# Performance work log

Measured on AMD Instinct MI355X. Metric: run time of the kernel, lower is better.

Reference implementation:

```python
import jax, jax.numpy as jnp
import numpy as np

EPS = 1e-10  # faithful to original: masked scores are set to eps, not -inf


def setup_inputs() -> dict:
    key = jax.random.key(0)
    ks = jax.random.split(key, 5)
    B, S, D, N, H = 2, 2048, 1024, 16, 64
    init_range = 0.02
    residual = jax.random.normal(ks[0], (B, S, D), dtype=jnp.float32)
    W_key = jax.random.normal(ks[1], (N, D, H), dtype=jnp.float32) * init_range
    W_query = jax.random.normal(ks[2], (N, D, H), dtype=jnp.float32) * init_range
    W_values = jax.random.normal(ks[3], (N, D, H), dtype=jnp.float32) * init_range
    W_output = jax.random.normal(ks[4], (N, H, D), dtype=jnp.float32) * init_range
    return {
        "residual": residual,
        "W_key": W_key, "W_query": W_query, "W_values": W_values, "W_output": W_output,
        "Bias_key": jnp.zeros((N, H), jnp.float32),
        "Bias_query": jnp.zeros((N, H), jnp.float32),
        "Bias_values": jnp.zeros((N, H), jnp.float32),
        "Bias_output": jnp.zeros((D,), jnp.float32),
    }


def reference(residual, W_key, W_query, W_values, W_output,
              Bias_key, Bias_query, Bias_values, Bias_output):
    B, S, D = residual.shape
    N, _, H = W_key.shape
    # projections: [b,s,n,h]
    keys = jnp.einsum('bse,neh->bsnh', residual, W_key) + Bias_key
    queries = jnp.einsum('bse,neh->bsnh', residual, W_query) + Bias_query
    values = jnp.einsum('bse,neh->bsnh', residual, W_values) + Bias_values
    # scores: [b,n,q,k]
    scores = jnp.einsum('bknh,bqnh->bnqk', keys, queries) / jnp.sqrt(jnp.asarray(H, scores_dtype(residual)))
    q_idx = jnp.arange(S)[:, None]
    k_idx = jnp.arange(S)[None, :]
    causal_mask = q_idx < k_idx  # future positions
    # QUIRK of original module: masked scores are assigned eps (~0), not -inf
    scores = jnp.where(causal_mask[None, None, :, :], jnp.asarray(EPS, scores.dtype), scores)
    probs = jax.nn.softmax(scores, axis=3)
    weighted = jnp.einsum('bnqk,bknh->bqnh', probs, values)
    out = jnp.einsum('bqnh,nhe->bqe', weighted, W_output) + Bias_output
    return out


def scores_dtype(x):
    return x.dtype
```

## Files before the change

kernel.cpp:

```cpp
#include <hip/hip_runtime.h>
#include <hip/hip_bf16.h>
#include <cmath>

typedef __bf16 bf16;
typedef __attribute__((ext_vector_type(4))) __bf16 bf16x4;
typedef __attribute__((ext_vector_type(8))) __bf16 bf16x8;
typedef __attribute__((ext_vector_type(4))) float f32x4;

#define B_ 2
#define S_ 2048
#define D_ 1024
#define N_ 16
#define H_ 64
#define LOG2E 1.44269504088896340736f

__device__ __forceinline__ void gload16(const bf16* g, bf16* l) {
  __builtin_amdgcn_global_load_lds(
      (const __attribute__((address_space(1))) void*)(g),
      (__attribute__((address_space(3))) void*)(l), 16, 0, 0);
}

__device__ __forceinline__ f32x4 mfma16(bf16x8 a, bf16x8 b, f32x4 c) {
  return __builtin_amdgcn_mfma_f32_16x16x32_bf16(a, b, c, 0, 0, 0);
}

__device__ __forceinline__ f32x4 zero4() {
  f32x4 v = {0.0f, 0.0f, 0.0f, 0.0f};
  return v;
}

__global__ __launch_bounds__(256) void cvt_kernel(
    const float* __restrict__ in, bf16* __restrict__ out, int n8) {
  int id = blockIdx.x * 256 + threadIdx.x;
  if (id >= n8) return;
  const float4* p = (const float4*)(in + (size_t)id * 8);
  float4 v0 = p[0], v1 = p[1];
  bf16x8 o;
  o[0] = (bf16)v0.x; o[1] = (bf16)v0.y; o[2] = (bf16)v0.z; o[3] = (bf16)v0.w;
  o[4] = (bf16)v1.x; o[5] = (bf16)v1.y; o[6] = (bf16)v1.z; o[7] = (bf16)v1.w;
  *(bf16x8*)(out + (size_t)id * 8) = o;
}

__global__ __launch_bounds__(256) void qkvw_transpose_kernel(
    const float* __restrict__ Wk, const float* __restrict__ Wq,
    const float* __restrict__ Wv, bf16* __restrict__ out) {
  __shared__ bf16 t[64][72];
  const int z = blockIdx.z;
  const float* W = (z < 16) ? Wk : (z < 32) ? Wq : Wv;
  const float* ing = W + (size_t)(z & 15) * (1024 * 64);
  bf16* outg = out + (size_t)z * (64 * 1024);
  const int r0 = blockIdx.x * 64;
  const int t8 = threadIdx.x & 7, trow = threadIdx.x >> 3;
#pragma unroll
  for (int p = 0; p < 2; ++p) {
    int r = trow + p * 32;
    const float4* src = (const float4*)(ing + (size_t)(r0 + r) * 64 + t8 * 8);
    float4 v0 = src[0], v1 = src[1];
    bf16x8 o;
    o[0] = (bf16)v0.x; o[1] = (bf16)v0.y; o[2] = (bf16)v0.z; o[3] = (bf16)v0.w;
    o[4] = (bf16)v1.x; o[5] = (bf16)v1.y; o[6] = (bf16)v1.z; o[7] = (bf16)v1.w;
    *(bf16x8*)(&t[r][t8 * 8]) = o;
  }
  __syncthreads();
#pragma unroll
  for (int p = 0; p < 2; ++p) {
    int c = trow + p * 32;
    bf16x8 v;
#pragma unroll
    for (int j = 0; j < 8; ++j) v[j] = t[t8 * 8 + j][c];
    *(bf16x8*)(outg + (size_t)c * 1024 + r0 + t8 * 8) = v;
  }
}

__global__ __launch_bounds__(256) void transpose_f32bf16_kernel(
    const float* __restrict__ in, bf16* __restrict__ out, int R, int C) {
  __shared__ bf16 t[64][72];
  const size_t mat = (size_t)R * C;
  const float* ing = in + (size_t)blockIdx.z * mat;
  bf16* outg = out + (size_t)blockIdx.z * mat;
  const int r0 = blockIdx.x * 64, c0 = blockIdx.y * 64;
  const int t8 = threadIdx.x & 7, trow = threadIdx.x >> 3;
#pragma unroll
  for (int p = 0; p < 2; ++p) {
    int r = trow + p * 32;
    const float4* src = (const float4*)(ing + (size_t)(r0 + r) * C + c0 + t8 * 8);
    float4 v0 = src[0], v1 = src[1];
    bf16x8 o;
    o[0] = (bf16)v0.x; o[1] = (bf16)v0.y; o[2] = (bf16)v0.z; o[3] = (bf16)v0.w;
    o[4] = (bf16)v1.x; o[5] = (bf16)v1.y; o[6] = (bf16)v1.z; o[7] = (bf16)v1.w;
    *(bf16x8*)(&t[r][t8 * 8]) = o;
  }
  __syncthreads();
#pragma unroll
  for (int p = 0; p < 2; ++p) {
    int c = trow + p * 32;
    bf16x8 v;
#pragma unroll
    for (int j = 0; j < 8; ++j) v[j] = t[t8 * 8 + j][c];
    *(bf16x8*)(outg + (size_t)(c0 + c) * R + r0 + t8 * 8) = v;
  }
}

__global__ __launch_bounds__(256) void transpose_bf16_kernel(
    const bf16* __restrict__ in, bf16* __restrict__ out, int R, int C) {
  __shared__ bf16 t[64][72];
  const size_t mat = (size_t)R * C;
  const bf16* ing = in + (size_t)blockIdx.z * mat;
  bf16* outg = out + (size_t)blockIdx.z * mat;
  const int r0 = blockIdx.x * 64, c0 = blockIdx.y * 64;
  const int t8 = threadIdx.x & 7, trow = threadIdx.x >> 3;
#pragma unroll
  for (int p = 0; p < 2; ++p) {
    int r = trow + p * 32;
    bf16x8 v = *(const bf16x8*)(ing + (size_t)(r0 + r) * C + c0 + t8 * 8);
    *(bf16x8*)(&t[r][t8 * 8]) = v;
  }
  __syncthreads();
#pragma unroll
  for (int p = 0; p < 2; ++p) {
    int c = trow + p * 32;
    bf16x8 v;
#pragma unroll
    for (int j = 0; j < 8; ++j) v[j] = t[t8 * 8 + j][c];
    *(bf16x8*)(outg + (size_t)(c0 + c) * R + r0 + t8 * 8) = v;
  }
}

__global__ __launch_bounds__(256) void sufv_tot_kernel(
    const bf16* __restrict__ Vp, float* __restrict__ tot) {
  __shared__ float red[4][64];
  const int hd = blockIdx.x, seg = blockIdx.y;
  const int h = threadIdx.x & 63, sub = threadIdx.x >> 6;
  const bf16* Vh = Vp + (size_t)hd * S_ * H_;
  float a = 0.0f;
  const int k0 = seg * 32 + sub * 8;
#pragma unroll
  for (int k = 0; k < 8; ++k) a += (float)Vh[(size_t)(k0 + k) * H_ + h];
  red[sub][h] = a;
  __syncthreads();
  if (sub == 0)
    tot[(hd * 64 + seg) * 64 + h] = red[0][h] + red[1][h] + red[2][h] + red[3][h];
}

__global__ __launch_bounds__(64) void sufv_scan_kernel(
    bf16* __restrict__ VS, const float* __restrict__ tot) {
  const int hd = blockIdx.x, seg = blockIdx.y, h = threadIdx.x;
  bf16* Vh = VS + (size_t)hd * S_ * H_;
  float a = 0.0f;
  for (int s2 = seg + 1; s2 < 64; ++s2) a += tot[(hd * 64 + s2) * 64 + h];
  for (int k = seg * 32 + 31; k >= seg * 32; --k) {
    const float v = (float)Vh[(size_t)k * H_ + h];
    Vh[(size_t)k * H_ + h] = (bf16)a;
    a += v;
  }
}

__global__ __launch_bounds__(512) void gemm_proj_kernel(
    const bf16* __restrict__ A, const bf16* __restrict__ Bt,
    const float* __restrict__ bk, const float* __restrict__ bq,
    const float* __restrict__ bv, bf16* __restrict__ proj_base) {
  __shared__ bf16 As[2][2][256 * 32];
  __shared__ bf16 Bs[2][2][256 * 32];
  const int tid = threadIdx.x;
  const int w = tid >> 6, l = tid & 63, lan = l & 15, grp = l >> 4;
  const int wm128 = (w >> 2) * 128, wn64 = (w & 3) * 64;
  const int m0 = blockIdx.y * 256, n0 = blockIdx.x * 256;
  const int zc = n0 >> 10;
  const float* bias = (zc == 0) ? bk : (zc == 1 ? bq : bv);
  bf16* Out = proj_base + (size_t)zc * ((size_t)B_ * N_ * S_ * H_);
  const int posx = (grp ^ ((lan >> 1) & 3)) << 3;

#define STG(LDS_, GP_, rb_, buf_, kh_, kb_)                                    \
  do {                                                                         \
    _Pragma("unroll") for (int jj = 0; jj < 2; ++jj) {                         \
      const int ci = jj * 512 + tid;                                           \
      const int rw = ci >> 2, cp = ci & 3;                                     \
      const int gg = cp ^ ((rw >> 1) & 3);                                     \
      gload16(GP_ + (size_t)((rb_) + rw) * 1024 + (kb_) + (kh_) * 32 + gg * 8, \
              &LDS_[buf_][kh_][(jj * 512 + w * 64) * 8]);                      \
    }                                                                          \
  } while (0)

  f32x4 acc[8][4];
#pragma unroll
  for (int i = 0; i < 8; ++i)
#pragma unroll
    for (int jv = 0; jv < 4; ++jv) acc[i][jv] = zero4();

  bf16x8 b[4];

#define DO_PHASE(buf_, mq_, kk_, READB_)                                       \
  do {                                                                         \
    if (READB_) {                                                              \
      _Pragma("unroll") for (int nf = 0; nf < 4; ++nf)                         \
        b[nf] = *(const bf16x8*)(&Bs[buf_][kk_][(wn64 + nf * 16 + lan) * 32 + posx]); \
    }                                                                          \
    bf16x8 a[4];                                                               \
    _Pragma("unroll") for (int mf = 0; mf < 4; ++mf)                           \
      a[mf] = *(const bf16x8*)(&As[buf_][kk_][(wm128 + (mq_) * 64 + mf * 16 + lan) * 32 + posx]); \
    __builtin_amdgcn_s_setprio(1);                                             \
    _Pragma("unroll") for (int mf = 0; mf < 4; ++mf)                           \
      _Pragma("unroll") for (int nf = 0; nf < 4; ++nf)                         \
        acc[(mq_) * 4 + mf][nf] = mfma16(a[mf], b[nf], acc[(mq_) * 4 + mf][nf]); \
    __builtin_amdgcn_s_setprio(0);                                             \
  } while (0)

  STG(As, A, m0, 0, 0, 0);
  STG(Bs, Bt, n0, 0, 0, 0);
  STG(As, A, m0, 0, 1, 0);
  STG(Bs, Bt, n0, 0, 1, 0);

  for (int t = 0; t < 15; ++t) {
    const int buf = t & 1;
    const int nkb = (t + 1) * 64;
    STG(As, A, m0, buf ^ 1, 0, nkb);
    asm volatile("s_waitcnt vmcnt(6)" ::: "memory");
    __builtin_amdgcn_s_barrier();
    asm volatile("" ::: "memory");
    DO_PHASE(buf, 0, 0, true);
    STG(Bs, Bt, n0, buf ^ 1, 0, nkb);
    asm volatile("" ::: "memory");
    __builtin_amdgcn_s_barrier();
    asm volatile("" ::: "memory");
    DO_PHASE(buf, 1, 0, false);
    STG(As, A, m0, buf ^ 1, 1, nkb);
    asm volatile("s_waitcnt vmcnt(6)" ::: "memory");
    __builtin_amdgcn_s_barrier();
    asm volatile("" ::: "memory");
    DO_PHASE(buf, 0, 1, true);
    STG(Bs, Bt, n0, buf ^ 1, 1, nkb);
    asm volatile("" ::: "memory");
    __builtin_amdgcn_s_barrier();
    asm volatile("" ::: "memory");
    DO_PHASE(buf, 1, 1, false);
  }
  {
    asm volatile("s_waitcnt vmcnt(4)" ::: "memory");
    __builtin_amdgcn_s_barrier();
    asm volatile("" ::: "memory");
    DO_PHASE(1, 0, 0, true);
    DO_PHASE(1, 1, 0, false);
    asm volatile("s_waitcnt vmcnt(0)" ::: "memory");
    __builtin_amdgcn_s_barrier();
    asm volatile("" ::: "memory");
    DO_PHASE(1, 0, 1, true);
    DO_PHASE(1, 1, 1, false);
  }
#undef STG
#undef DO_PHASE

#pragma unroll
  for (int nf = 0; nf < 4; ++nf) {
    const int c10 = (n0 + wn64 + nf * 16 + lan) & 1023;
    const float bs = bias[c10];
    const int n = c10 >> 6, h = c10 & 63;
#pragma unroll
    for (int am = 0; am < 8; ++am) {
#pragma unroll
      for (int r = 0; r < 4; ++r) {
        const int m = m0 + wm128 + am * 16 + grp * 4 + r;
        const int bb = m >> 11, s = m & 2047;
        Out[((size_t)((bb * N_ + n) * S_ + s)) * H_ + h] = (bf16)(acc[am][nf][r] + bs);
      }
    }
  }
}

__global__ __launch_bounds__(256) void gemm_out_kernel(
    const bf16* __restrict__ A, const bf16* __restrict__ Bt,
    const float* __restrict__ bias, float* __restrict__ Out) {
  __shared__ bf16 As[128 * 64];
  __shared__ bf16 Bs[128 * 64];
  const int tid = threadIdx.x;
  const int w = tid >> 6, l = tid & 63, lan = l & 15, grp = l >> 4;
  const int mb = (w >> 1) * 64, nb = (w & 1) * 64;
  const int m0 = blockIdx.y * 128, n0 = blockIdx.x * 128;
  const int lrow8 = l >> 3;
  const int swl = ((l & 7) ^ lrow8) * 8;
  const int l7 = lan & 7;

  f32x4 acc[4][4];
#pragma unroll
  for (int i = 0; i < 4; ++i)
#pragma unroll
    for (int j = 0; j < 4; ++j) acc[i][j] = zero4();

  for (int kb = 0; kb < 1024; kb += 64) {
    __syncthreads();
#pragma unroll
    for (int i = 0; i < 4; ++i) {
      int ch = w * 4 + i;
      gload16(A + (size_t)(m0 + ch * 8 + lrow8) * 1024 + kb + swl, As + ch * 512);
      gload16(Bt + (size_t)(n0 + ch * 8 + lrow8) * 1024 + kb + swl, Bs + ch * 512);
    }
    __syncthreads();
#pragma unroll
    for (int kk = 0; kk < 2; ++kk) {
      bf16x8 a[4], b[4];
#pragma unroll
      for (int mf = 0; mf < 4; ++mf)
        a[mf] = *(const bf16x8*)(As + (mb + mf * 16 + lan) * 64 + (((grp + kk * 4) ^ l7) << 3));
#pragma unroll
      for (int nf = 0; nf < 4; ++nf)
        b[nf] = *(const bf16x8*)(Bs + (nb + nf * 16 + lan) * 64 + (((grp + kk * 4) ^ l7) << 3));
#pragma unroll
      for (int mf = 0; mf < 4; ++mf)
#pragma unroll
        for (int nf = 0; nf < 4; ++nf)
          acc[mf][nf] = mfma16(a[mf], b[nf], acc[mf][nf]);
    }
  }
#pragma unroll
  for (int nf = 0; nf < 4; ++nf) {
    int c = n0 + nb + nf * 16 + lan;
    float bs = bias[c];
#pragma unroll
    for (int mf = 0; mf < 4; ++mf) {
#pragma unroll
      for (int r = 0; r < 4; ++r) {
        int m = m0 + mb + mf * 16 + grp * 4 + r;
        Out[(size_t)m * 1024 + c] = acc[mf][nf][r] + bs;
      }
    }
  }
}

__global__ __launch_bounds__(256) void attn_kernel(
    const bf16* __restrict__ Qp, const bf16* __restrict__ Kp,
    const bf16* __restrict__ Vt, const bf16* __restrict__ Suf,
    bf16* __restrict__ Wtd, float* __restrict__ PoA, float* __restrict__ PoB,
    float* __restrict__ PpA, float* __restrict__ PpB) {
  __shared__ bf16 Ks[2][64 * 64];
  __shared__ bf16 Vs[2][64 * 64];
  __shared__ bf16 Ps[4][32 * 72];
  const int tid = threadIdx.x;
  const int w = tid >> 6, l = tid & 63, lan = l & 15, grp = l >> 4;
  const int bi = blockIdx.x;
  const int qq = bi >> 8;
  const int j = bi & 255;
  const int hd = j & 31, wv = j >> 5;
  int x, t0, t1;
  if (qq == 0)      { x = 15 - wv; t0 = 0;     t1 = x + 1; }
  else if (qq == 1) { x = 15 - wv; t0 = x + 1; t1 = 2 * x + 2; }
  else              { x = wv;      t0 = 0;     t1 = 2 * x + 2; }
  const int qw = x * 128 + w * 32;
  const bf16* Qh = Qp + (size_t)hd * S_ * H_;
  const bf16* Kh = Kp + (size_t)hd * S_ * H_;
  const bf16* Vh = Vt + (size_t)hd * H_ * S_;
  const bf16* Sufh = Suf + (size_t)hd * S_ * H_;
  const int lrow8 = l >> 3;
  const int swl = ((l & 7) ^ lrow8) * 8;
  const int l7 = lan & 7;
  const float cexp = 0.125f * LOG2E;

#define STAGE(buf, kb_)                                                        \
  do {                                                                         \
    _Pragma("unroll") for (int i2 = 0; i2 < 2; ++i2) {                         \
      int ch = w * 2 + i2;                                                     \
      gload16(Kh + (size_t)((kb_) + ch * 8 + lrow8) * H_ + swl,                \
              &Ks[buf][ch * 512]);                                             \
      gload16(Vh + (size_t)(ch * 8 + lrow8) * S_ + (kb_) + swl,                \
              &Vs[buf][ch * 512]);                                             \
    }                                                                          \
  } while (0)

  bf16x8 qa[2][2];
#pragma unroll
  for (int qt = 0; qt < 2; ++qt)
#pragma unroll
    for (int kf = 0; kf < 2; ++kf)
      qa[qt][kf] = *(const bf16x8*)(Qh + (size_t)(qw + qt * 16 + lan) * H_ + grp * 8 + kf * 32);

  f32x4 o[2][4];
  float psum[2] = {0.0f, 0.0f};
#pragma unroll
  for (int qt = 0; qt < 2; ++qt)
#pragma unroll
    for (int hf = 0; hf < 4; ++hf) o[qt][hf] = zero4();

  bf16* Pw = &Ps[w][0];

  STAGE(0, t0 * 64);
  for (int tt = t0; tt < t1; ++tt) {
    const int kb = tt * 64;
    const int cur = (tt - t0) & 1;
    if (tt + 1 < t1) {
      STAGE(cur ^ 1, kb + 64);
      asm volatile("s_waitcnt vmcnt(4)" ::: "memory");
    } else {
      asm volatile("s_waitcnt vmcnt(0)" ::: "memory");
    }
    __builtin_amdgcn_s_barrier();

    if (kb <= qw + 31) {
      const bf16* Kc = &Ks[cur][0];
      const bf16* Vc = &Vs[cur][0];

      f32x4 s2[4][2];
#pragma unroll
      for (int k2 = 0; k2 < 4; ++k2)
#pragma unroll
        for (int qt = 0; qt < 2; ++qt) s2[k2][qt] = zero4();
      __builtin_amdgcn_s_setprio(1);
#pragma unroll
      for (int kf = 0; kf < 2; ++kf) {
        bf16x8 kfr[4];
#pragma unroll
        for (int k2 = 0; k2 < 4; ++k2)
          kfr[k2] = *(const bf16x8*)(Kc + (k2 * 16 + lan) * 64 + (((grp + kf * 4) ^ l7) << 3));
#pragma unroll
        for (int k2 = 0; k2 < 4; ++k2)
#pragma unroll
          for (int qt = 0; qt < 2; ++qt)
            s2[k2][qt] = mfma16(kfr[k2], qa[qt][kf], s2[k2][qt]);
      }
      __builtin_amdgcn_s_setprio(0);

      const bool maskt = (kb + 63 > qw);
#pragma unroll
      for (int qt = 0; qt < 2; ++qt) {
        const int q_g = qw + qt * 16 + lan;
#pragma unroll
        for (int k2 = 0; k2 < 4; ++k2) {
          f32x4 p;
#pragma unroll
          for (int r = 0; r < 4; ++r) p[r] = exp2f(s2[k2][qt][r] * cexp);
          if (maskt) {
            const int kg0 = kb + k2 * 16 + grp * 4;
#pragma unroll
            for (int r = 0; r < 4; ++r)
              if (kg0 + r > q_g) p[r] = 0.0f;
          }
          psum[qt] += (p[0] + p[1]) + (p[2] + p[3]);
          unsigned plo, phi;
          asm("v_cvt_pk_bf16_f32 %0, %1, %2" : "=v"(plo) : "v"(p[0]), "v"(p[1]));
          asm("v_cvt_pk_bf16_f32 %0, %1, %2" : "=v"(phi) : "v"(p[2]), "v"(p[3]));
          uint2 u; u.x = plo; u.y = phi;
          *(uint2*)(Pw + (qt * 16 + lan) * 72 + k2 * 16 + grp * 4) = u;
        }
      }

      __builtin_amdgcn_s_setprio(1);
#pragma unroll
      for (int ks = 0; ks < 2; ++ks) {
        bf16x8 pa[2], vb[4];
#pragma unroll
        for (int qt = 0; qt < 2; ++qt)
          pa[qt] = *(const bf16x8*)(Pw + (qt * 16 + lan) * 72 + grp * 8 + ks * 32);
#pragma unroll
        for (int hf = 0; hf < 4; ++hf)
          vb[hf] = *(const bf16x8*)(Vc + (hf * 16 + lan) * 64 + (((grp + ks * 4) ^ l7) << 3));
#pragma unroll
        for (int qt = 0; qt < 2; ++qt)
#pragma unroll
          for (int hf = 0; hf < 4; ++hf)
            o[qt][hf] = mfma16(pa[qt], vb[hf], o[qt][hf]);
      }
      __builtin_amdgcn_s_setprio(0);
    }
    __builtin_amdgcn_s_barrier();
  }
#undef STAGE

#pragma unroll
  for (int qt = 0; qt < 2; ++qt) {
    psum[qt] += __shfl_xor(psum[qt], 16);
    psum[qt] += __shfl_xor(psum[qt], 32);
  }

  if (qq == 2) {
    const size_t outbase = (size_t)(hd >> 4) * S_ * (N_ * H_) + (size_t)(hd & 15) * H_;
#pragma unroll
    for (int qt = 0; qt < 2; ++qt) {
#pragma unroll
      for (int r = 0; r < 4; ++r) {
        const int q_g = qw + qt * 16 + grp * 4 + r;
        const float ps = __shfl(psum[qt], grp * 4 + r);
        const float inv = 1.0f / (ps + (float)(2047 - q_g));
#pragma unroll
        for (int hf = 0; hf < 4; ++hf) {
          const int h = hf * 16 + lan;
          const float suf = (float)Sufh[(size_t)q_g * H_ + h];
          Wtd[outbase + (size_t)q_g * (N_ * H_) + h] = (bf16)((o[qt][hf][r] + suf) * inv);
        }
      }
    }
  } else {
    float* Po = (qq == 0) ? PoA : PoB;
    float* Pp = (qq == 0) ? PpA : PpB;
    const int pb = (hd * 8 + (x - 8)) * 128 + w * 32;
#pragma unroll
    for (int qt = 0; qt < 2; ++qt) {
#pragma unroll
      for (int r = 0; r < 4; ++r) {
        const int rl = qt * 16 + grp * 4 + r;
        const float ps = __shfl(psum[qt], grp * 4 + r);
        if (lan == 0) Pp[pb + rl] = ps;
#pragma unroll
        for (int hf = 0; hf < 4; ++hf)
          Po[(size_t)(pb + rl) * 64 + hf * 16 + lan] = o[qt][hf][r];
      }
    }
  }
}

__global__ __launch_bounds__(256) void combine_kernel(
    const float* __restrict__ PoA, const float* __restrict__ PoB,
    const float* __restrict__ PpA, const float* __restrict__ PpB,
    const bf16* __restrict__ Suf, bf16* __restrict__ Wtd) {
  const int hd = blockIdx.x >> 3, xi = blockIdx.x & 7;
  const int x = xi + 8;
  const int pb = (hd * 8 + xi) * 128;
  const size_t outbase = (size_t)(hd >> 4) * S_ * (N_ * H_) + (size_t)(hd & 15) * H_;
#pragma unroll
  for (int it = 0; it < 8; ++it) {
    const int e = it * 256 + threadIdx.x;
    const int rl = e >> 4, h4 = (e & 15) * 4;
    const int q_g = x * 128 + rl;
    const float Z = PpA[pb + rl] + PpB[pb + rl] + (float)(2047 - q_g);
    const float inv = 1.0f / Z;
    const float4 a = *(const float4*)(PoA + (size_t)(pb + rl) * 64 + h4);
    const float4 b = *(const float4*)(PoB + (size_t)(pb + rl) * 64 + h4);
    const bf16x4 s4 = *(const bf16x4*)(Suf + ((size_t)hd * S_ + q_g) * 64 + h4);
    bf16x4 ov;
    ov[0] = (bf16)((a.x + b.x + (float)s4[0]) * inv);
    ov[1] = (bf16)((a.y + b.y + (float)s4[1]) * inv);
    ov[2] = (bf16)((a.z + b.z + (float)s4[2]) * inv);
    ov[3] = (bf16)((a.w + b.w + (float)s4[3]) * inv);
    *(bf16x4*)(Wtd + outbase + (size_t)q_g * (N_ * H_) + h4) = ov;
  }
}

extern "C" void kernel_launch(void* const* d_in, const int* in_sizes, int n_in,
                              void* d_out, int out_size, void* d_ws, size_t ws_size,
                              hipStream_t stream) {
  const float* residual = (const float*)d_in[0];
  const float* Wk = (const float*)d_in[1];
  const float* Wq = (const float*)d_in[2];
  const float* Wv = (const float*)d_in[3];
  const float* Wo = (const float*)d_in[4];
  const float* Bk = (const float*)d_in[5];
  const float* Bq = (const float*)d_in[6];
  const float* Bv = (const float*)d_in[7];
  const float* Bo = (const float*)d_in[8];
  float* outp = (float*)d_out;

  char* ws = (char*)d_ws;
  const size_t MB = 1024 * 1024;
  bf16* Abf = (bf16*)(ws + 0 * MB);
  bf16* Wot = (bf16*)(ws + 8 * MB);
  bf16* Wkt = (bf16*)(ws + 10 * MB);
  bf16* Kp  = (bf16*)(ws + 16 * MB);
  bf16* Qp  = (bf16*)(ws + 24 * MB);
  bf16* Vp  = (bf16*)(ws + 32 * MB);
  bf16* Vtp = (bf16*)(ws + 40 * MB);
  bf16* Wtd = Abf;
  float* PpA = (float*)(ws + 10 * MB);
  float* PpB = (float*)(ws + 10 * MB + 128 * 1024);
  float* tot = (float*)(ws + 10 * MB + 256 * 1024);
  bf16* Suf = Vp;
  float* PoA = (float*)d_out;
  float* PoB = (float*)d_out + 2 * 1024 * 1024;
  (void)in_sizes; (void)n_in; (void)out_size; (void)ws_size;

  cvt_kernel<<<2048, 256, 0, stream>>>(residual, Abf, (B_ * S_ * D_) / 8);

  qkvw_transpose_kernel<<<dim3(16, 1, 48), 256, 0, stream>>>(Wk, Wq, Wv, Wkt);
  transpose_f32bf16_kernel<<<dim3(16, 16, 1), 256, 0, stream>>>(Wo, Wot, 1024, 1024);

  gemm_proj_kernel<<<dim3(12, 16), 512, 0, stream>>>(Abf, Wkt, Bk, Bq, Bv, Kp);

  sufv_tot_kernel<<<dim3(32, 64), 256, 0, stream>>>(Vp, tot);
  transpose_bf16_kernel<<<dim3(32, 1, 32), 256, 0, stream>>>(Vp, Vtp, 2048, 64);
  sufv_scan_kernel<<<dim3(32, 64), 64, 0, stream>>>(Vp, tot);

  attn_kernel<<<768, 256, 0, stream>>>(Qp, Kp, Vtp, Suf, Wtd, PoA, PoB, PpA, PpB);

  combine_kernel<<<256, 256, 0, stream>>>(PoA, PoB, PpA, PpB, Suf, Wtd);

  gemm_out_kernel<<<dim3(8, 32, 1), 256, 0, stream>>>(Wtd, Wot, Bo, outp);
}
```

Before: 149.0 us.

## Merge prep and V-processing kernels, remap GEMM block indices across XCDs

```diff
diff --git a/kernel.cpp b/kernel.cpp
--- a/kernel.cpp
+++ b/kernel.cpp
@@ -29,56 +29,34 @@
   return v;
 }
 
-__global__ __launch_bounds__(256) void cvt_kernel(
-    const float* __restrict__ in, bf16* __restrict__ out, int n8) {
-  int id = blockIdx.x * 256 + threadIdx.x;
-  if (id >= n8) return;
-  const float4* p = (const float4*)(in + (size_t)id * 8);
-  float4 v0 = p[0], v1 = p[1];
-  bf16x8 o;
-  o[0] = (bf16)v0.x; o[1] = (bf16)v0.y; o[2] = (bf16)v0.z; o[3] = (bf16)v0.w;
-  o[4] = (bf16)v1.x; o[5] = (bf16)v1.y; o[6] = (bf16)v1.z; o[7] = (bf16)v1.w;
-  *(bf16x8*)(out + (size_t)id * 8) = o;
-}
-
-__global__ __launch_bounds__(256) void qkvw_transpose_kernel(
+__global__ __launch_bounds__(256) void prep_kernel(
+    const float* __restrict__ residual, bf16* __restrict__ Abf,
     const float* __restrict__ Wk, const float* __restrict__ Wq,
-    const float* __restrict__ Wv, bf16* __restrict__ out) {
+    const float* __restrict__ Wv, bf16* __restrict__ Wkt,
+    const float* __restrict__ Wo, bf16* __restrict__ Wot) {
   __shared__ bf16 t[64][72];
-  const int z = blockIdx.z;
-  const float* W = (z < 16) ? Wk : (z < 32) ? Wq : Wv;
-  const float* ing = W + (size_t)(z & 15) * (1024 * 64);
-  bf16* outg = out + (size_t)z * (64 * 1024);
-  const int r0 = blockIdx.x * 64;
-  const int t8 = threadIdx.x & 7, trow = threadIdx.x >> 3;
-#pragma unroll
-  for (int p = 0; p < 2; ++p) {
-    int r = trow + p * 32;
-    const float4* src = (const float4*)(ing + (size_t)(r0 + r) * 64 + t8 * 8);
-    float4 v0 = src[0], v1 = src[1];
+  const int bi = blockIdx.x;
+  if (bi < 2048) {
+    const int id = bi * 256 + threadIdx.x;
+    const float4* p = (const float4*)(residual + (size_t)id * 8);
+    float4 v0 = p[0], v1 = p[1];
     bf16x8 o;
     o[0] = (bf16)v0.x; o[1] = (bf16)v0.y; o[2] = (bf16)v0.z; o[3] = (bf16)v0.w;
     o[4] = (bf16)v1.x; o[5] = (bf16)v1.y; o[6] = (bf16)v1.z; o[7] = (bf16)v1.w;
-    *(bf16x8*)(&t[r][t8 * 8]) = o;
-  }
-  __syncthreads();
-#pragma unroll
-  for (int p = 0; p < 2; ++p) {
-    int c = trow + p * 32;
-    bf16x8 v;
-#pragma unroll
-    for (int j = 0; j < 8; ++j) v[j] = t[t8 * 8 + j][c];
-    *(bf16x8*)(outg + (size_t)c * 1024 + r0 + t8 * 8) = v;
-  }
-}
-
-__global__ __launch_bounds__(256) void transpose_f32bf16_kernel(
-    const float* __restrict__ in, bf16* __restrict__ out, int R, int C) {
-  __shared__ bf16 t[64][72];
-  const size_t mat = (size_t)R * C;
-  const float* ing = in + (size_t)blockIdx.z * mat;
-  bf16* outg = out + (size_t)blockIdx.z * mat;
-  const int r0 = blockIdx.x * 64, c0 = blockIdx.y * 64;
+    *(bf16x8*)(Abf + (size_t)id * 8) = o;
+    return;
+  }
+  const float* ing; bf16* outg; int C, r0, c0;
+  if (bi < 2816) {
+    const int idx = bi - 2048, z = idx >> 4, xr = idx & 15;
+    const float* W = (z < 16) ? Wk : (z < 32) ? Wq : Wv;
+    ing = W + (size_t)(z & 15) * (1024 * 64);
+    outg = Wkt + (size_t)z * (64 * 1024);
+    C = 64; r0 = xr * 64; c0 = 0;
+  } else {
+    const int idx = bi - 2816, xr = idx & 15, yc = idx >> 4;
+    ing = Wo; outg = Wot; C = 1024; r0 = xr * 64; c0 = yc * 64;
+  }
   const int t8 = threadIdx.x & 7, trow = threadIdx.x >> 3;
 #pragma unroll
   for (int p = 0; p < 2; ++p) {
@@ -97,22 +75,39 @@
     bf16x8 v;
 #pragma unroll
     for (int j = 0; j < 8; ++j) v[j] = t[t8 * 8 + j][c];
-    *(bf16x8*)(outg + (size_t)(c0 + c) * R + r0 + t8 * 8) = v;
-  }
-}
-
-__global__ __launch_bounds__(256) void transpose_bf16_kernel(
-    const bf16* __restrict__ in, bf16* __restrict__ out, int R, int C) {
+    *(bf16x8*)(outg + (size_t)(c0 + c) * 1024 + r0 + t8 * 8) = v;
+  }
+}
+
+__global__ __launch_bounds__(256) void vwork_kernel(
+    const bf16* __restrict__ Vp, float* __restrict__ tot,
+    bf16* __restrict__ Vtp) {
   __shared__ bf16 t[64][72];
-  const size_t mat = (size_t)R * C;
-  const bf16* ing = in + (size_t)blockIdx.z * mat;
-  bf16* outg = out + (size_t)blockIdx.z * mat;
-  const int r0 = blockIdx.x * 64, c0 = blockIdx.y * 64;
+  __shared__ float red[4][64];
+  const int bi = blockIdx.x;
+  if (bi < 2048) {
+    const int hd = bi >> 6, seg = bi & 63;
+    const int h = threadIdx.x & 63, sub = threadIdx.x >> 6;
+    const bf16* Vh = Vp + (size_t)hd * S_ * H_;
+    float a = 0.0f;
+    const int k0 = seg * 32 + sub * 8;
+#pragma unroll
+    for (int k = 0; k < 8; ++k) a += (float)Vh[(size_t)(k0 + k) * H_ + h];
+    red[sub][h] = a;
+    __syncthreads();
+    if (sub == 0)
+      tot[(hd * 64 + seg) * 64 + h] = red[0][h] + red[1][h] + red[2][h] + red[3][h];
+    return;
+  }
+  const int idx = bi - 2048, z = idx >> 5, xr = idx & 31;
+  const bf16* ing = Vp + (size_t)z * (S_ * H_);
+  bf16* outg = Vtp + (size_t)z * (S_ * H_);
+  const int r0 = xr * 64;
   const int t8 = threadIdx.x & 7, trow = threadIdx.x >> 3;
 #pragma unroll
   for (int p = 0; p < 2; ++p) {
     int r = trow + p * 32;
-    bf16x8 v = *(const bf16x8*)(ing + (size_t)(r0 + r) * C + c0 + t8 * 8);
+    bf16x8 v = *(const bf16x8*)(ing + (size_t)(r0 + r) * 64 + t8 * 8);
     *(bf16x8*)(&t[r][t8 * 8]) = v;
   }
   __syncthreads();
@@ -122,24 +117,8 @@
     bf16x8 v;
 #pragma unroll
     for (int j = 0; j < 8; ++j) v[j] = t[t8 * 8 + j][c];
-    *(bf16x8*)(outg + (size_t)(c0 + c) * R + r0 + t8 * 8) = v;
-  }
-}
-
-__global__ __launch_bounds__(256) void sufv_tot_kernel(
-    const bf16* __restrict__ Vp, float* __restrict__ tot) {
-  __shared__ float red[4][64];
-  const int hd = blockIdx.x, seg = blockIdx.y;
-  const int h = threadIdx.x & 63, sub = threadIdx.x >> 6;
-  const bf16* Vh = Vp + (size_t)hd * S_ * H_;
-  float a = 0.0f;
-  const int k0 = seg * 32 + sub * 8;
-#pragma unroll
-  for (int k = 0; k < 8; ++k) a += (float)Vh[(size_t)(k0 + k) * H_ + h];
-  red[sub][h] = a;
-  __syncthreads();
-  if (sub == 0)
-    tot[(hd * 64 + seg) * 64 + h] = red[0][h] + red[1][h] + red[2][h] + red[3][h];
+    *(bf16x8*)(outg + (size_t)c * 2048 + r0 + t8 * 8) = v;
+  }
 }
 
 __global__ __launch_bounds__(64) void sufv_scan_kernel(
@@ -164,7 +143,9 @@
   const int tid = threadIdx.x;
   const int w = tid >> 6, l = tid & 63, lan = l & 15, grp = l >> 4;
   const int wm128 = (w >> 2) * 128, wn64 = (w & 3) * 64;
-  const int m0 = blockIdx.y * 256, n0 = blockIdx.x * 256;
+  const int bid = blockIdx.x;
+  const int bid2 = (bid & 7) * 24 + (bid >> 3);
+  const int m0 = (bid2 / 12) * 256, n0 = (bid2 % 12) * 256;
   const int zc = n0 >> 10;
   const float* bias = (zc == 0) ? bk : (zc == 1 ? bq : bv);
   bf16* Out = proj_base + (size_t)zc * ((size_t)B_ * N_ * S_ * H_);
@@ -274,7 +255,9 @@
   const int tid = threadIdx.x;
   const int w = tid >> 6, l = tid & 63, lan = l & 15, grp = l >> 4;
   const int mb = (w >> 1) * 64, nb = (w & 1) * 64;
-  const int m0 = blockIdx.y * 128, n0 = blockIdx.x * 128;
+  const int bid = blockIdx.x;
+  const int bid2 = (bid & 7) * 32 + (bid >> 3);
+  const int m0 = (bid2 >> 3) * 128, n0 = (bid2 & 7) * 128;
   const int lrow8 = l >> 3;
   const int swl = ((l & 7) ^ lrow8) * 8;
   const int l7 = lan & 7;
@@ -563,20 +546,17 @@
   float* PoB = (float*)d_out + 2 * 1024 * 1024;
   (void)in_sizes; (void)n_in; (void)out_size; (void)ws_size;
 
-  cvt_kernel<<<2048, 256, 0, stream>>>(residual, Abf, (B_ * S_ * D_) / 8);
-
-  qkvw_transpose_kernel<<<dim3(16, 1, 48), 256, 0, stream>>>(Wk, Wq, Wv, Wkt);
-  transpose_f32bf16_kernel<<<dim3(16, 16, 1), 256, 0, stream>>>(Wo, Wot, 1024, 1024);
-
-  gemm_proj_kernel<<<dim3(12, 16), 512, 0, stream>>>(Abf, Wkt, Bk, Bq, Bv, Kp);
-
-  sufv_tot_kernel<<<dim3(32, 64), 256, 0, stream>>>(Vp, tot);
-  transpose_bf16_kernel<<<dim3(32, 1, 32), 256, 0, stream>>>(Vp, Vtp, 2048, 64);
+  prep_kernel<<<3072, 256, 0, stream>>>(residual, Abf, Wk, Wq, Wv, Wkt, Wo, Wot);
+
+  gemm_proj_kernel<<<192, 512, 0, stream>>>(Abf, Wkt, Bk, Bq, Bv, Kp);
+
+  vwork_kernel<<<3072, 256, 0, stream>>>(Vp, tot, Vtp);
+
   sufv_scan_kernel<<<dim3(32, 64), 64, 0, stream>>>(Vp, tot);
 
   attn_kernel<<<768, 256, 0, stream>>>(Qp, Kp, Vtp, Suf, Wtd, PoA, PoB, PpA, PpB);
 
   combine_kernel<<<256, 256, 0, stream>>>(PoA, PoB, PpA, PpB, Suf, Wtd);
 
-  gemm_out_kernel<<<dim3(8, 32, 1), 256, 0, stream>>>(Wtd, Wot, Bo, outp);
-}
+  gemm_out_kernel<<<256, 256, 0, stream>>>(Wtd, Wot, Bo, outp);
+}
```

New measurement: 149.5 us. No clear change (+0.3%).
